# Performance work log

Measured on AMD Instinct MI355X. Metric: run time of the kernel, lower is better.

## Reference

```python
import jax, jax.numpy as jnp
import numpy as np

H = 16        # num_attention_heads
D = 1024      # hidden_size
HD = D // H   # head_dim = 64


def setup_inputs() -> dict:
    key = jax.random.key(0)
    ks = jax.random.split(key, 5)
    B, T = 16, 1024
    s_in = 1.0 / np.sqrt(D)
    return {
        "hidden_states": jax.random.normal(ks[0], (B, T, D), dtype=jnp.float32),
        "w_qkv": jax.random.normal(ks[1], (D, 3 * D), dtype=jnp.float32) * s_in,
        "b_qkv": jnp.zeros((3 * D,), dtype=jnp.float32),
        "w_out": jax.random.normal(ks[2], (D, D), dtype=jnp.float32) * s_in,
        "b_out": jnp.zeros((D,), dtype=jnp.float32),
    }


def reference(hidden_states, w_qkv, b_qkv, w_out, b_out):
    B, T, C = hidden_states.shape
    qkv = hidden_states @ w_qkv + b_qkv                      # [B,T,3C]
    q, k, v = jnp.split(qkv, 3, axis=-1)
    # [B,T,C] -> [B,H,T,HD]
    q = q.reshape(B, T, H, HD).transpose(0, 2, 1, 3)
    k = k.reshape(B, T, H, HD).transpose(0, 2, 1, 3)
    v = v.reshape(B, T, H, HD).transpose(0, 2, 1, 3)
    scale = 1.0 / np.sqrt(HD)
    logits = jnp.einsum("bhqd,bhkd->bhqk", q, k) * scale     # [B,H,T,T]
    attn = jax.nn.softmax(logits, axis=-1)
    out = jnp.einsum("bhqk,bhkd->bhqd", attn, v)             # [B,H,T,HD]
    out = out.transpose(0, 2, 1, 3).reshape(B, T, C)
    return out @ w_out + b_out
```

## Files before the change

kernel.cpp:

```cpp
#include <hip/hip_runtime.h>
#include <cstdint>
#include <cstddef>

typedef _Float16 h8 __attribute__((ext_vector_type(8)));
typedef _Float16 h4 __attribute__((ext_vector_type(4)));
typedef float f4 __attribute__((ext_vector_type(4)));

#define MFMA(a, b, c) __builtin_amdgcn_mfma_f32_16x16x32_f16((a), (b), (c), 0, 0, 0)

__device__ __forceinline__ void gl_lds16(const void* g, void* l) {
  __builtin_amdgcn_global_load_lds((const __attribute__((address_space(1))) void*)g,
                                   (__attribute__((address_space(3))) void*)l, 16, 0, 0);
}

__device__ __forceinline__ h8 lds_frag(const char* base, int r, int ch) {
  return *(const h8*)(base + ((r * 8 + (ch ^ (r & 7))) * 16));
}

__device__ __forceinline__ void BAR() {
  asm volatile("" ::: "memory");
  __builtin_amdgcn_s_barrier();
  asm volatile("" ::: "memory");
}

__global__ void k_cvt_hs(const float* __restrict__ in, _Float16* __restrict__ out, int n8) {
  int i = blockIdx.x * blockDim.x + threadIdx.x;
  if (i >= n8) return;
  size_t idx = (size_t)i * 8;
  float4 a = *(const float4*)(in + idx);
  float4 b = *(const float4*)(in + idx + 4);
  h8 o;
  o[0] = (_Float16)a.x; o[1] = (_Float16)a.y; o[2] = (_Float16)a.z; o[3] = (_Float16)a.w;
  o[4] = (_Float16)b.x; o[5] = (_Float16)b.y; o[6] = (_Float16)b.z; o[7] = (_Float16)b.w;
  *(h8*)(out + idx) = o;
}

__global__ void k_transcvt(const float* __restrict__ in, _Float16* __restrict__ out, int N, int K) {
  __shared__ float tile[64 * 65];
  int tn = blockIdx.x * 64, tk = blockIdx.y * 64;
  for (int i = 0; i < 4; ++i) {
    int cid = i * 256 + threadIdx.x;
    int r = cid >> 4, c4 = cid & 15;
    float4 v = *(const float4*)(in + (size_t)(tk + r) * N + tn + c4 * 4);
    tile[r * 65 + c4 * 4 + 0] = v.x; tile[r * 65 + c4 * 4 + 1] = v.y;
    tile[r * 65 + c4 * 4 + 2] = v.z; tile[r * 65 + c4 * 4 + 3] = v.w;
  }
  __syncthreads();
  for (int i = 0; i < 2; ++i) {
    int cid = i * 256 + threadIdx.x;
    int n = cid >> 3, kc = cid & 7;
    h8 o;
    for (int j = 0; j < 8; ++j) o[j] = (_Float16)tile[(kc * 8 + j) * 65 + n];
    *(h8*)(out + (size_t)(tn + n) * K + tk + kc * 8) = o;
  }
}

__device__ __forceinline__ void gemm256_mainloop(
    const _Float16* __restrict__ A, const _Float16* __restrict__ BT,
    char* smem, int tm, int tn, f4 (&acc)[8][4]) {
  int tid = threadIdx.x, lane = tid & 63, wave = tid >> 6;
  int l15 = lane & 15, l4 = lane >> 4;
  int wm = (wave >> 2) * 128, wn = (wave & 3) * 64;
  const _Float16* Ab = A + (size_t)tm * 1024;
  const _Float16* Bb = BT + (size_t)tn * 1024;
  int r0 = tid >> 3, cg = (tid & 7) ^ (r0 & 7);
  char* cA = smem;           char* nA = smem + 32768;
  char* cB = smem + 65536;   char* nB = smem + 98304;

  auto stA = [&](int kt, int h, char* dst) {
    const _Float16* s = Ab + (size_t)(h * 128 + r0) * 1024 + kt + cg * 8;
    gl_lds16(s, dst + h * 16384 + tid * 16);
    gl_lds16(s + 64 * 1024, dst + h * 16384 + 8192 + tid * 16);
  };
  auto stB = [&](int kt, int h, char* dst) {
    const _Float16* s = Bb + (size_t)(h * 128 + r0) * 1024 + kt + cg * 8;
    gl_lds16(s, dst + h * 16384 + tid * 16);
    gl_lds16(s + 64 * 1024, dst + h * 16384 + 8192 + tid * 16);
  };

  stA(0, 0, cA); stA(0, 1, cA);
  stB(0, 0, cB); stB(0, 1, cB);
  stB(64, 0, nB); stB(64, 1, nB);
  asm volatile("s_waitcnt vmcnt(4)" ::: "memory");
  BAR();

  h8 af[4][2], bf[4][2];
  for (int u = 0; u < 16; ++u) {
    int kt1 = (u + 1) << 6, kt2 = (u + 2) << 6;
#pragma unroll
    for (int mi = 0; mi < 4; ++mi) {
      int r = wm + mi * 16 + l15;
      af[mi][0] = lds_frag(cA, r, l4);
      af[mi][1] = lds_frag(cA, r, 4 + l4);
    }
#pragma unroll
    for (int nj = 0; nj < 2; ++nj) {
      int r = wn + nj * 16 + l15;
      bf[nj][0] = lds_frag(cB, r, l4);
      bf[nj][1] = lds_frag(cB, r, 4 + l4);
    }
    if (u < 15) stA(kt1, 0, nA);
    asm volatile("s_waitcnt lgkmcnt(8)" ::: "memory");
    BAR();
    asm volatile("s_waitcnt lgkmcnt(0)" ::: "memory");
    __builtin_amdgcn_s_setprio(1);
#pragma unroll
    for (int kk = 0; kk < 2; ++kk)
#pragma unroll
      for (int mi = 0; mi < 4; ++mi)
#pragma unroll
        for (int nj = 0; nj < 2; ++nj)
          acc[mi][nj] = MFMA(af[mi][kk], bf[nj][kk], acc[mi][nj]);
    __builtin_amdgcn_s_setprio(0);
    BAR();
#pragma unroll
    for (int nj = 2; nj < 4; ++nj) {
      int r = wn + nj * 16 + l15;
      bf[nj][0] = lds_frag(cB, r, l4);
      bf[nj][1] = lds_frag(cB, r, 4 + l4);
    }
    if (u < 15) stA(kt1, 1, nA);
    BAR();
    asm volatile("s_waitcnt lgkmcnt(0)" ::: "memory");
    __builtin_amdgcn_s_setprio(1);
#pragma unroll
    for (int kk = 0; kk < 2; ++kk)
#pragma unroll
      for (int mi = 0; mi < 4; ++mi)
#pragma unroll
        for (int nj = 2; nj < 4; ++nj)
          acc[mi][nj] = MFMA(af[mi][kk], bf[nj][kk], acc[mi][nj]);
    __builtin_amdgcn_s_setprio(0);
    BAR();
#pragma unroll
    for (int mi = 0; mi < 4; ++mi) {
      int r = wm + 64 + mi * 16 + l15;
      af[mi][0] = lds_frag(cA, r, l4);
      af[mi][1] = lds_frag(cA, r, 4 + l4);
    }
    if (u < 14) stB(kt2, 0, cB);
    BAR();
    asm volatile("s_waitcnt lgkmcnt(0)" ::: "memory");
    __builtin_amdgcn_s_setprio(1);
#pragma unroll
    for (int kk = 0; kk < 2; ++kk)
#pragma unroll
      for (int mi = 0; mi < 4; ++mi)
#pragma unroll
        for (int nj = 2; nj < 4; ++nj)
          acc[4 + mi][nj] = MFMA(af[mi][kk], bf[nj][kk], acc[4 + mi][nj]);
    __builtin_amdgcn_s_setprio(0);
    BAR();
    if (u < 14) stB(kt2, 1, cB);
    if (u < 14) asm volatile("s_waitcnt vmcnt(4)" ::: "memory");
    else        asm volatile("s_waitcnt vmcnt(0)" ::: "memory");
    BAR();
    __builtin_amdgcn_s_setprio(1);
#pragma unroll
    for (int kk = 0; kk < 2; ++kk)
#pragma unroll
      for (int mi = 0; mi < 4; ++mi)
#pragma unroll
        for (int nj = 0; nj < 2; ++nj)
          acc[4 + mi][nj] = MFMA(af[mi][kk], bf[nj][kk], acc[4 + mi][nj]);
    __builtin_amdgcn_s_setprio(0);
    BAR();
    char* t = cA; cA = nA; nA = t;
    t = cB; cB = nB; nB = t;
  }
}

__global__ __launch_bounds__(512) void k_gemm_qkv(
    const _Float16* __restrict__ A, const _Float16* __restrict__ BT,
    const float* __restrict__ bias,
    _Float16* __restrict__ Q, _Float16* __restrict__ Kq, _Float16* __restrict__ Vt) {
  __shared__ char smem[131072];
  int id = blockIdx.x;
  int swz = (id & 7) * 96 + (id >> 3);
  int by = swz / 12, bx = swz - by * 12;
  int tm = by * 256, tn = bx * 256;
  f4 acc[8][4] = {};
  gemm256_mainloop(A, BT, smem, tm, tn, acc);

  int tid = threadIdx.x, lane = tid & 63, wave = tid >> 6;
  int l15 = lane & 15, l4 = lane >> 4;
  int wm = (wave >> 2) * 128, wn = (wave & 3) * 64;
  if (tn < 2048) {
    _Float16* dst = (tn >= 1024) ? Kq : Q;
#pragma unroll
    for (int nj = 0; nj < 4; ++nj) {
      int n = tn + wn + nj * 16 + l15;
      float bv = bias[n];
      int h = (n >> 6) & 15, d = n & 63;
#pragma unroll
      for (int mig = 0; mig < 8; ++mig) {
#pragma unroll
        for (int r = 0; r < 4; ++r) {
          int m = tm + wm + mig * 16 + l4 * 4 + r;
          int b = m >> 10, t = m & 1023;
          dst[(((size_t)b * 16 + h) * 1024 + t) * 64 + d] =
              (_Float16)(acc[mig][nj][r] + bv);
        }
      }
    }
  } else {
    _Float16* L = (_Float16*)smem;
    int b = tm >> 10, tb = tm & 1023;
#pragma unroll
    for (int p = 0; p < 2; ++p) {
      __syncthreads();
      if (((wave >> 1) & 1) == p) {
        int nloc = (wave & 1) * 64;
#pragma unroll
        for (int nj = 0; nj < 4; ++nj) {
          int nl = nloc + nj * 16 + l15;
          float bv = bias[tn + p * 128 + nl];
#pragma unroll
          for (int mig = 0; mig < 8; ++mig) {
            h4 pk;
#pragma unroll
            for (int r = 0; r < 4; ++r) pk[r] = (_Float16)(acc[mig][nj][r] + bv);
            *(h4*)(L + nl * 264 + wm + mig * 16 + l4 * 4) = pk;
          }
        }
      }
      __syncthreads();
#pragma unroll
      for (int i = 0; i < 8; ++i) {
        int cid = i * 512 + tid;
        int nl = cid >> 5, tc = cid & 31;
        int ng = tn + p * 128 + nl;
        int h = (ng >> 6) & 15, d = ng & 63;
        *(h8*)(Vt + (((size_t)b * 16 + h) * 64 + d) * 1024 + tb + tc * 8) =
            *(const h8*)(L + nl * 264 + tc * 8);
      }
    }
  }
}

__global__ __launch_bounds__(256, 2) void k_attn(
    const _Float16* __restrict__ Q, const _Float16* __restrict__ Kk,
    const _Float16* __restrict__ Vt, _Float16* __restrict__ O) {
  __shared__ char smem[20480 + 32768];
  _Float16* sP = (_Float16*)smem;
  char* sKV = smem + 20480;
  const float SCL = 0.125f * 1.44269504088896340736f;
  int tid = threadIdx.x, wave = tid >> 6, lane = tid & 63;
  int l15 = lane & 15, l4 = lane >> 4;
  int bh = blockIdx.y;
  int qt = blockIdx.x * 256;
  const _Float16* Qb = Q + (size_t)bh * 65536;
  const _Float16* Kb = Kk + (size_t)bh * 65536;
  const _Float16* Vb = Vt + (size_t)bh * 65536;

  h8 qf[4][2];
#pragma unroll
  for (int nt = 0; nt < 4; ++nt) {
    int r = qt + wave * 64 + nt * 16 + l15;
#pragma unroll
    for (int kk = 0; kk < 2; ++kk)
      qf[nt][kk] = *(const h8*)(Qb + (size_t)r * 64 + (kk * 4 + l4) * 8);
  }
  _Float16 scl_h = (_Float16)SCL;
#pragma unroll
  for (int nt = 0; nt < 4; ++nt)
#pragma unroll
    for (int kk = 0; kk < 2; ++kk)
#pragma unroll
      for (int j = 0; j < 8; ++j) qf[nt][kk][j] *= scl_h;

  int cid0 = tid, cid1 = tid + 256;
  int r0 = cid0 >> 3, c0 = (cid0 & 7) ^ (r0 & 7);
  int r1 = cid1 >> 3, c1 = (cid1 & 7) ^ (r1 & 7);
  const _Float16* kp0 = Kb + (size_t)r0 * 64 + c0 * 8;
  const _Float16* kp1 = Kb + (size_t)r1 * 64 + c1 * 8;
  const _Float16* vp0 = Vb + (size_t)r0 * 1024 + c0 * 8;
  const _Float16* vp1 = Vb + (size_t)r1 * 1024 + c1 * 8;

  auto stage = [&](int it, int b) {
    char* dK = sKV + b * 16384;
    char* dV = dK + 8192;
    size_t ko = (size_t)it * 4096;
    size_t vo = (size_t)it * 64;
    gl_lds16(kp0 + ko, dK + cid0 * 16);
    gl_lds16(kp1 + ko, dK + cid1 * 16);
    gl_lds16(vp0 + vo, dV + cid0 * 16);
    gl_lds16(vp1 + vo, dV + cid1 * 16);
  };

  f4 oacc[4][4] = {};
  f4 lacc[4] = {};
  h8 ones;
#pragma unroll
  for (int j = 0; j < 8; ++j) ones[j] = (_Float16)1.0f;
  _Float16* pw = sP + wave * 64 * 40;

  stage(0, 0);
  asm volatile("s_waitcnt vmcnt(0)" ::: "memory");
  BAR();

  for (int it = 0; it < 16; ++it) {
    int cur = it & 1;
    if (it < 15) stage(it + 1, cur ^ 1);
    const char* sK = sKV + cur * 16384;
    const char* sV = sK + 8192;
    for (int mh = 0; mh < 2; ++mh) {
      f4 sacc[2][4] = {};
#pragma unroll
      for (int kk = 0; kk < 2; ++kk) {
        h8 kf[2];
        int ch = kk * 4 + l4;
#pragma unroll
        for (int mt = 0; mt < 2; ++mt) {
          int r = mh * 32 + mt * 16 + l15;
          kf[mt] = *(const h8*)(sK + ((r * 8 + (ch ^ (r & 7))) * 16));
        }
#pragma unroll
        for (int mt = 0; mt < 2; ++mt)
#pragma unroll
          for (int nt = 0; nt < 4; ++nt)
            sacc[mt][nt] = MFMA(kf[mt], qf[nt][kk], sacc[mt][nt]);
      }
#pragma unroll
      for (int mt = 0; mt < 2; ++mt) {
#pragma unroll
        for (int nt = 0; nt < 4; ++nt) {
          float p0 = exp2f(sacc[mt][nt][0]);
          float p1 = exp2f(sacc[mt][nt][1]);
          float p2 = exp2f(sacc[mt][nt][2]);
          float p3 = exp2f(sacc[mt][nt][3]);
          h4 pk;
          pk[0] = (_Float16)p0; pk[1] = (_Float16)p1;
          pk[2] = (_Float16)p2; pk[3] = (_Float16)p3;
          *(h4*)(pw + (nt * 16 + l15) * 40 + mt * 16 + l4 * 4) = pk;
        }
      }
      h8 pf[4], vf[4];
#pragma unroll
      for (int mi = 0; mi < 4; ++mi)
        pf[mi] = *(const h8*)(pw + (mi * 16 + l15) * 40 + l4 * 8);
      int ch = mh * 4 + l4;
#pragma unroll
      for (int nd = 0; nd < 4; ++nd) {
        int r = nd * 16 + l15;
        vf[nd] = *(const h8*)(sV + ((r * 8 + (ch ^ (r & 7))) * 16));
      }
#pragma unroll
      for (int mi = 0; mi < 4; ++mi) {
#pragma unroll
        for (int nd = 0; nd < 4; ++nd)
          oacc[mi][nd] = MFMA(pf[mi], vf[nd], oacc[mi][nd]);
        lacc[mi] = MFMA(pf[mi], ones, lacc[mi]);
      }
    }
    asm volatile("s_waitcnt vmcnt(0) lgkmcnt(0)" ::: "memory");
    BAR();
  }
  int b = bh >> 4, h = bh & 15;
#pragma unroll
  for (int mi = 0; mi < 4; ++mi) {
#pragma unroll
    for (int r = 0; r < 4; ++r) {
      float inv = 1.f / lacc[mi][r];
      int t = qt + wave * 64 + mi * 16 + l4 * 4 + r;
#pragma unroll
      for (int nd = 0; nd < 4; ++nd)
        O[(size_t)(b * 1024 + t) * 1024 + h * 64 + nd * 16 + l15] =
            (_Float16)(oacc[mi][nd][r] * inv);
    }
  }
}

__global__ __launch_bounds__(512) void k_gemm_out(
    const _Float16* __restrict__ A, const _Float16* __restrict__ BT,
    const float* __restrict__ bias, float* __restrict__ C) {
  __shared__ char smem[131072];
  int id = blockIdx.x;
  int swz = (id & 7) * 32 + (id >> 3);
  int by = swz >> 2, bx = swz & 3;
  int tm = by * 256, tn = bx * 256;
  f4 acc[8][4] = {};
  gemm256_mainloop(A, BT, smem, tm, tn, acc);

  int tid = threadIdx.x, lane = tid & 63, wave = tid >> 6;
  int l15 = lane & 15, l4 = lane >> 4;
  int wm = (wave >> 2) * 128, wn = (wave & 3) * 64;
#pragma unroll
  for (int nj = 0; nj < 4; ++nj) {
    int n = tn + wn + nj * 16 + l15;
    float bv = bias[n];
#pragma unroll
    for (int mig = 0; mig < 8; ++mig) {
#pragma unroll
      for (int r = 0; r < 4; ++r) {
        int m = tm + wm + mig * 16 + l4 * 4 + r;
        C[(size_t)m * 1024 + n] = acc[mig][nj][r] + bv;
      }
    }
  }
}

extern "C" void kernel_launch(void* const* d_in, const int* in_sizes, int n_in,
                              void* d_out, int out_size, void* d_ws, size_t ws_size,
                              hipStream_t stream) {
  const float* hs    = (const float*)d_in[0];
  const float* w_qkv = (const float*)d_in[1];
  const float* b_qkv = (const float*)d_in[2];
  const float* w_out = (const float*)d_in[3];
  const float* b_out = (const float*)d_in[4];
  float* out = (float*)d_out;
  char* ws = (char*)d_ws;

  _Float16* hs_h  = (_Float16*)(ws);
  _Float16* wqkvT = (_Float16*)(ws + 33554432);
  _Float16* woutT = (_Float16*)(ws + 39845888);
  _Float16* q_ws  = (_Float16*)(ws + 41943040);
  _Float16* k_ws  = (_Float16*)(ws + 75497472);
  _Float16* vt_ws = (_Float16*)(ws + 109051904);

  k_cvt_hs<<<8192, 256, 0, stream>>>(hs, hs_h, 2097152);
  k_transcvt<<<dim3(48, 16), 256, 0, stream>>>(w_qkv, wqkvT, 3072, 1024);
  k_transcvt<<<dim3(16, 16), 256, 0, stream>>>(w_out, woutT, 1024, 1024);
  k_gemm_qkv<<<768, 512, 0, stream>>>(hs_h, wqkvT, b_qkv, q_ws, k_ws, vt_ws);
  _Float16* attn_h = hs_h;
  k_attn<<<dim3(4, 256), 256, 0, stream>>>(q_ws, k_ws, vt_ws, attn_h);
  k_gemm_out<<<256, 512, 0, stream>>>(attn_h, woutT, b_out, out);
}
```

Measured before the change: 397.6 us.

## Make QKV GEMM blocks loop over Q/K/V tiles with cross-tile prefetch

The QKV projection GEMM now launches 256 blocks instead of 768. Each block keeps one A row-panel and computes its Q, K and V output tiles in turn. Loads for the next tile's first k-steps are issued during the last iterations of the current tile, hiding the pipeline prologue and reusing A from cache. The attention softmax now uses the raw hardware exp2 builtin and packed round-toward-zero fp16 conversion, and an end-of-loop lgkmcnt wait is dropped. These changes add pipeline-state complexity and slightly change rounding of the probabilities.

Result: faster. 359.2 us (-9.7%).

```diff
diff --git a/kernel.cpp b/kernel.cpp
--- a/kernel.cpp
+++ b/kernel.cpp
@@ -4,6 +4,7 @@
 
 typedef _Float16 h8 __attribute__((ext_vector_type(8)));
 typedef _Float16 h4 __attribute__((ext_vector_type(4)));
+typedef __fp16 fp16x2 __attribute__((ext_vector_type(2)));
 typedef float f4 __attribute__((ext_vector_type(4)));
 
 #define MFMA(a, b, c) __builtin_amdgcn_mfma_f32_16x16x32_f16((a), (b), (c), 0, 0, 0)
@@ -55,34 +56,36 @@
   }
 }
 
-__device__ __forceinline__ void gemm256_mainloop(
-    const _Float16* __restrict__ A, const _Float16* __restrict__ BT,
-    char* smem, int tm, int tn, f4 (&acc)[8][4]) {
+__device__ __forceinline__ void gemm256_tile(
+    const _Float16* __restrict__ Ab, const _Float16* __restrict__ Bb,
+    const _Float16* __restrict__ BbN, bool first, bool more,
+    char* smem, f4 (&acc)[8][4]) {
+  constexpr int TILE = 32768, HALF = 16384;
   int tid = threadIdx.x, lane = tid & 63, wave = tid >> 6;
   int l15 = lane & 15, l4 = lane >> 4;
   int wm = (wave >> 2) * 128, wn = (wave & 3) * 64;
-  const _Float16* Ab = A + (size_t)tm * 1024;
-  const _Float16* Bb = BT + (size_t)tn * 1024;
-  int r0 = tid >> 3, cg = (tid & 7) ^ (r0 & 7);
-  char* cA = smem;           char* nA = smem + 32768;
-  char* cB = smem + 65536;   char* nB = smem + 98304;
+  int rs = tid >> 3, cg = (tid & 7) ^ (rs & 7);
+  char* cA = smem;            char* nA = smem + TILE;
+  char* cB = smem + 2 * TILE; char* nB = smem + 3 * TILE;
 
   auto stA = [&](int kt, int h, char* dst) {
-    const _Float16* s = Ab + (size_t)(h * 128 + r0) * 1024 + kt + cg * 8;
-    gl_lds16(s, dst + h * 16384 + tid * 16);
-    gl_lds16(s + 64 * 1024, dst + h * 16384 + 8192 + tid * 16);
+    const _Float16* s = Ab + (size_t)(h * 128 + rs) * 1024 + kt + cg * 8;
+    gl_lds16(s, dst + h * HALF + tid * 16);
+    gl_lds16(s + (size_t)64 * 1024, dst + h * HALF + 8192 + tid * 16);
   };
-  auto stB = [&](int kt, int h, char* dst) {
-    const _Float16* s = Bb + (size_t)(h * 128 + r0) * 1024 + kt + cg * 8;
-    gl_lds16(s, dst + h * 16384 + tid * 16);
-    gl_lds16(s + 64 * 1024, dst + h * 16384 + 8192 + tid * 16);
+  auto stB = [&](const _Float16* base, int kt, int h, char* dst) {
+    const _Float16* s = base + (size_t)(h * 128 + rs) * 1024 + kt + cg * 8;
+    gl_lds16(s, dst + h * HALF + tid * 16);
+    gl_lds16(s + (size_t)64 * 1024, dst + h * HALF + 8192 + tid * 16);
   };
 
-  stA(0, 0, cA); stA(0, 1, cA);
-  stB(0, 0, cB); stB(0, 1, cB);
-  stB(64, 0, nB); stB(64, 1, nB);
-  asm volatile("s_waitcnt vmcnt(4)" ::: "memory");
-  BAR();
+  if (first) {
+    stA(0, 0, cA); stA(0, 1, cA);
+    stB(Bb, 0, 0, cB); stB(Bb, 0, 1, cB);
+    stB(Bb, 64, 0, nB); stB(Bb, 64, 1, nB);
+    asm volatile("s_waitcnt vmcnt(4)" ::: "memory");
+    BAR();
+  }
 
   h8 af[4][2], bf[4][2];
   for (int u = 0; u < 16; ++u) {
@@ -100,6 +103,7 @@
       bf[nj][1] = lds_frag(cB, r, 4 + l4);
     }
     if (u < 15) stA(kt1, 0, nA);
+    else if (more) stA(0, 0, nA);
     asm volatile("s_waitcnt lgkmcnt(8)" ::: "memory");
     BAR();
     asm volatile("s_waitcnt lgkmcnt(0)" ::: "memory");
@@ -120,6 +124,7 @@
       bf[nj][1] = lds_frag(cB, r, 4 + l4);
     }
     if (u < 15) stA(kt1, 1, nA);
+    else if (more) stA(0, 1, nA);
     BAR();
     asm volatile("s_waitcnt lgkmcnt(0)" ::: "memory");
     __builtin_amdgcn_s_setprio(1);
@@ -138,7 +143,8 @@
       af[mi][0] = lds_frag(cA, r, l4);
       af[mi][1] = lds_frag(cA, r, 4 + l4);
     }
-    if (u < 14) stB(kt2, 0, cB);
+    if (u < 14) stB(Bb, kt2, 0, cB);
+    else if (more) stB(BbN, (u == 14) ? 0 : 64, 0, cB);
     BAR();
     asm volatile("s_waitcnt lgkmcnt(0)" ::: "memory");
     __builtin_amdgcn_s_setprio(1);
@@ -151,9 +157,10 @@
           acc[4 + mi][nj] = MFMA(af[mi][kk], bf[nj][kk], acc[4 + mi][nj]);
     __builtin_amdgcn_s_setprio(0);
     BAR();
-    if (u < 14) stB(kt2, 1, cB);
-    if (u < 14) asm volatile("s_waitcnt vmcnt(4)" ::: "memory");
-    else        asm volatile("s_waitcnt vmcnt(0)" ::: "memory");
+    if (u < 14) stB(Bb, kt2, 1, cB);
+    else if (more) stB(BbN, (u == 14) ? 0 : 64, 1, cB);
+    if (u < 14 || more) asm volatile("s_waitcnt vmcnt(4)" ::: "memory");
+    else                asm volatile("s_waitcnt vmcnt(0)" ::: "memory");
     BAR();
     __builtin_amdgcn_s_setprio(1);
 #pragma unroll
@@ -176,63 +183,70 @@
     _Float16* __restrict__ Q, _Float16* __restrict__ Kq, _Float16* __restrict__ Vt) {
   __shared__ char smem[131072];
   int id = blockIdx.x;
-  int swz = (id & 7) * 96 + (id >> 3);
-  int by = swz / 12, bx = swz - by * 12;
-  int tm = by * 256, tn = bx * 256;
-  f4 acc[8][4] = {};
-  gemm256_mainloop(A, BT, smem, tm, tn, acc);
-
+  int swz = (id & 7) * 32 + (id >> 3);
+  int by = swz >> 2, c = swz & 3;
+  int tm = by * 256;
+  const _Float16* Ab = A + (size_t)tm * 1024;
   int tid = threadIdx.x, lane = tid & 63, wave = tid >> 6;
   int l15 = lane & 15, l4 = lane >> 4;
   int wm = (wave >> 2) * 128, wn = (wave & 3) * 64;
-  if (tn < 2048) {
-    _Float16* dst = (tn >= 1024) ? Kq : Q;
-#pragma unroll
-    for (int nj = 0; nj < 4; ++nj) {
-      int n = tn + wn + nj * 16 + l15;
-      float bv = bias[n];
-      int h = (n >> 6) & 15, d = n & 63;
-#pragma unroll
-      for (int mig = 0; mig < 8; ++mig) {
-#pragma unroll
-        for (int r = 0; r < 4; ++r) {
-          int m = tm + wm + mig * 16 + l4 * 4 + r;
-          int b = m >> 10, t = m & 1023;
-          dst[(((size_t)b * 16 + h) * 1024 + t) * 64 + d] =
-              (_Float16)(acc[mig][nj][r] + bv);
-        }
-      }
-    }
-  } else {
-    _Float16* L = (_Float16*)smem;
-    int b = tm >> 10, tb = tm & 1023;
-#pragma unroll
-    for (int p = 0; p < 2; ++p) {
-      __syncthreads();
-      if (((wave >> 1) & 1) == p) {
-        int nloc = (wave & 1) * 64;
-#pragma unroll
-        for (int nj = 0; nj < 4; ++nj) {
-          int nl = nloc + nj * 16 + l15;
-          float bv = bias[tn + p * 128 + nl];
-#pragma unroll
-          for (int mig = 0; mig < 8; ++mig) {
-            h4 pk;
-#pragma unroll
-            for (int r = 0; r < 4; ++r) pk[r] = (_Float16)(acc[mig][nj][r] + bv);
-            *(h4*)(L + nl * 264 + wm + mig * 16 + l4 * 4) = pk;
+
+  for (int t = 0; t < 3; ++t) {
+    int tn = (t * 4 + c) * 256;
+    const _Float16* Bb = BT + (size_t)tn * 1024;
+    const _Float16* BbN = Bb + (size_t)1024 * 1024;
+    f4 acc[8][4] = {};
+    gemm256_tile(Ab, Bb, BbN, t == 0, t < 2, smem, acc);
+
+    if (t < 2) {
+      _Float16* dst = (t == 0) ? Q : Kq;
+#pragma unroll
+      for (int nj = 0; nj < 4; ++nj) {
+        int n = tn + wn + nj * 16 + l15;
+        float bv = bias[n];
+        int h = (n >> 6) & 15, d = n & 63;
+#pragma unroll
+        for (int mig = 0; mig < 8; ++mig) {
+#pragma unroll
+          for (int r = 0; r < 4; ++r) {
+            int m = tm + wm + mig * 16 + l4 * 4 + r;
+            int b = m >> 10, tt = m & 1023;
+            dst[(((size_t)b * 16 + h) * 1024 + tt) * 64 + d] =
+                (_Float16)(acc[mig][nj][r] + bv);
           }
         }
       }
-      __syncthreads();
-#pragma unroll
-      for (int i = 0; i < 8; ++i) {
-        int cid = i * 512 + tid;
-        int nl = cid >> 5, tc = cid & 31;
-        int ng = tn + p * 128 + nl;
-        int h = (ng >> 6) & 15, d = ng & 63;
-        *(h8*)(Vt + (((size_t)b * 16 + h) * 64 + d) * 1024 + tb + tc * 8) =
-            *(const h8*)(L + nl * 264 + tc * 8);
+    } else {
+      _Float16* L = (_Float16*)smem;
+      int b = tm >> 10, tb = tm & 1023;
+#pragma unroll
+      for (int p = 0; p < 2; ++p) {
+        __syncthreads();
+        if (((wave >> 1) & 1) == p) {
+          int nloc = (wave & 1) * 64;
+#pragma unroll
+          for (int nj = 0; nj < 4; ++nj) {
+            int nl = nloc + nj * 16 + l15;
+            float bv = bias[tn + p * 128 + nl];
+#pragma unroll
+            for (int mig = 0; mig < 8; ++mig) {
+              h4 pk;
+#pragma unroll
+              for (int r = 0; r < 4; ++r) pk[r] = (_Float16)(acc[mig][nj][r] + bv);
+              *(h4*)(L + nl * 264 + wm + mig * 16 + l4 * 4) = pk;
+            }
+          }
+        }
+        __syncthreads();
+#pragma unroll
+        for (int i = 0; i < 8; ++i) {
+          int cid = i * 512 + tid;
+          int nl = cid >> 5, tc = cid & 31;
+          int ng = tn + p * 128 + nl;
+          int h = (ng >> 6) & 15, d = ng & 63;
+          *(h8*)(Vt + (((size_t)b * 16 + h) * 64 + d) * 1024 + tb + tc * 8) =
+              *(const h8*)(L + nl * 264 + tc * 8);
+        }
       }
     }
   }
@@ -325,14 +339,14 @@
       for (int mt = 0; mt < 2; ++mt) {
 #pragma unroll
         for (int nt = 0; nt < 4; ++nt) {
-          float p0 = exp2f(sacc[mt][nt][0]);
-          float p1 = exp2f(sacc[mt][nt][1]);
-          float p2 = exp2f(sacc[mt][nt][2]);
-          float p3 = exp2f(sacc[mt][nt][3]);
-          h4 pk;
-          pk[0] = (_Float16)p0; pk[1] = (_Float16)p1;
-          pk[2] = (_Float16)p2; pk[3] = (_Float16)p3;
-          *(h4*)(pw + (nt * 16 + l15) * 40 + mt * 16 + l4 * 4) = pk;
+          float p0 = __builtin_amdgcn_exp2f(sacc[mt][nt][0]);
+          float p1 = __builtin_amdgcn_exp2f(sacc[mt][nt][1]);
+          float p2 = __builtin_amdgcn_exp2f(sacc[mt][nt][2]);
+          float p3 = __builtin_amdgcn_exp2f(sacc[mt][nt][3]);
+          union { fp16x2 h[2]; h4 v; } uu;
+          uu.h[0] = __builtin_amdgcn_cvt_pkrtz(p0, p1);
+          uu.h[1] = __builtin_amdgcn_cvt_pkrtz(p2, p3);
+          *(h4*)(pw + (nt * 16 + l15) * 40 + mt * 16 + l4 * 4) = uu.v;
         }
       }
       h8 pf[4], vf[4];
@@ -353,7 +367,7 @@
         lacc[mi] = MFMA(pf[mi], ones, lacc[mi]);
       }
     }
-    asm volatile("s_waitcnt vmcnt(0) lgkmcnt(0)" ::: "memory");
+    asm volatile("s_waitcnt vmcnt(0)" ::: "memory");
     BAR();
   }
   int b = bh >> 4, h = bh & 15;
@@ -380,7 +394,8 @@
   int by = swz >> 2, bx = swz & 3;
   int tm = by * 256, tn = bx * 256;
   f4 acc[8][4] = {};
-  gemm256_mainloop(A, BT, smem, tm, tn, acc);
+  gemm256_tile(A + (size_t)tm * 1024, BT + (size_t)tn * 1024, nullptr,
+               true, false, smem, acc);
 
   int tid = threadIdx.x, lane = tid & 63, wave = tid >> 6;
   int l15 = lane & 15, l4 = lane >> 4;
@@ -421,7 +436,7 @@
   k_cvt_hs<<<8192, 256, 0, stream>>>(hs, hs_h, 2097152);
   k_transcvt<<<dim3(48, 16), 256, 0, stream>>>(w_qkv, wqkvT, 3072, 1024);
   k_transcvt<<<dim3(16, 16), 256, 0, stream>>>(w_out, woutT, 1024, 1024);
-  k_gemm_qkv<<<768, 512, 0, stream>>>(hs_h, wqkvT, b_qkv, q_ws, k_ws, vt_ws);
+  k_gemm_qkv<<<256, 512, 0, stream>>>(hs_h, wqkvT, b_qkv, q_ws, k_ws, vt_ws);
   _Float16* attn_h = hs_h;
   k_attn<<<dim3(4, 256), 256, 0, stream>>>(q_ws, k_ws, vt_ws, attn_h);
   k_gemm_out<<<256, 512, 0, stream>>>(attn_h, woutT, b_out, out);
```
